# Performance work log

Hardware: AMD Instinct MI355X
Metric: run time of the kernel (lower is better)

The kernel has to match this reference:

```python
import jax, jax.numpy as jnp
import numpy as np

B, S, D, H = 2, 512, 512, 8
HD = D // H  # 64


def setup_inputs() -> dict:
    key = jax.random.key(0)
    ks = jax.random.split(key, 14)
    sd = 1.0 / np.sqrt(D)
    sh = 1.0 / np.sqrt(HD)
    return {
        "query": jax.random.normal(ks[0], (B, S, D), jnp.float32),
        "key_": jax.random.normal(ks[1], (B, S, D), jnp.float32),
        "value": jax.random.normal(ks[2], (B, S, D), jnp.float32),
        "Wq": jax.random.uniform(ks[3], (D, D), jnp.float32, -sd, sd),
        "bq": jax.random.uniform(ks[4], (D,), jnp.float32, -sd, sd),
        "Wk": jax.random.uniform(ks[5], (D, D), jnp.float32, -sd, sd),
        "bk": jax.random.uniform(ks[6], (D,), jnp.float32, -sd, sd),
        "Wv": jax.random.uniform(ks[7], (D, D), jnp.float32, -sd, sd),
        "bv": jax.random.uniform(ks[8], (D,), jnp.float32, -sd, sd),
        "Wo": jax.random.uniform(ks[9], (D, D), jnp.float32, -sd, sd),
        "bo": jax.random.uniform(ks[10], (D,), jnp.float32, -sd, sd),
        "Aq": jax.random.uniform(ks[11], (HD, HD), jnp.float32, -sh, sh),
        "Ak": jax.random.uniform(ks[12], (HD, HD), jnp.float32, -sh, sh),
        "av": jax.random.normal(ks[13], (HD,), jnp.float32) * sh,
    }


def _heads(x):
    b, s, _ = x.shape
    return x.reshape(b, s, H, HD).transpose(0, 2, 1, 3)  # [b,h,s,hd]


def reference(query, key_, value, Wq, bq, Wk, bk, Wv, bv, Wo, bo, Aq, Ak, av):
    q = _heads(query @ Wq + bq)   # [b,h,q,hd]
    k = _heads(key_ @ Wk + bk)    # [b,h,k,hd]
    v = _heads(value @ Wv + bv)   # [b,h,k,hd]
    # additive (Bahdanau-style) scores: tanh(add_q(q)[:,:,:,None]+add_k(k)[:,:,None]) . av
    q_term = (q @ Aq)[:, :, :, None, :]   # [b,h,q,1,hd]
    k_term = (k @ Ak)[:, :, None, :, :]   # [b,h,1,k,hd]
    scores = jnp.einsum('bhqkd,d->bhqk', jnp.tanh(q_term + k_term), av)
    attn_weights = jax.nn.softmax(scores, axis=-1)  # dropout is identity at eval
    ctx = jnp.einsum('bhqk,bhkd->bhqd', attn_weights, v)
    b, _, s, _ = ctx.shape
    ctx = ctx.transpose(0, 2, 1, 3).reshape(b, s, D)
    out = ctx @ Wo + bo
    return out, attn_weights
```

## Files before the change

### kernel.cpp

```cpp
#include <hip/hip_runtime.h>
#include <math.h>

#define Bb 2
#define Ss 512
#define Dd 512
#define Hh 8
#define HDd 64
#define BS (Bb*Ss)

#if __has_builtin(__builtin_amdgcn_exp2f)
#define EXP2F(x) __builtin_amdgcn_exp2f(x)
#else
#define EXP2F(x) exp2f(x)
#endif
#if __has_builtin(__builtin_amdgcn_rcpf)
#define RCPF(x) __builtin_amdgcn_rcpf(x)
#else
#define RCPF(x) (1.0f/(x))
#endif

typedef float v4f __attribute__((ext_vector_type(4)));
typedef short v8s __attribute__((ext_vector_type(8)));

struct HL { short h, l; };

__device__ __forceinline__ HL split1(float x) {
  unsigned u = __builtin_bit_cast(unsigned, x);
  unsigned h = (u + 0x7fffu + ((u >> 16) & 1u)) >> 16;
  float hf = __builtin_bit_cast(float, h << 16);
  float lo = x - hf;
  unsigned ul = __builtin_bit_cast(unsigned, lo);
  unsigned l = (ul + 0x7fffu + ((ul >> 16) & 1u)) >> 16;
  HL r; r.h = (short)h; r.l = (short)l;
  return r;
}

__device__ __forceinline__ void split8p(const float* __restrict__ xp, v8s& ah, v8s& al) {
#pragma unroll
  for (int j = 0; j < 8; j++) {
    const HL r = split1(xp[j]);
    ah[j] = r.h; al[j] = r.l;
  }
}

__device__ __forceinline__ void split8v(float4 x0, float4 x1, v8s& ah, v8s& al) {
  HL r;
  r = split1(x0.x); ah[0] = r.h; al[0] = r.l;
  r = split1(x0.y); ah[1] = r.h; al[1] = r.l;
  r = split1(x0.z); ah[2] = r.h; al[2] = r.l;
  r = split1(x0.w); ah[3] = r.h; al[3] = r.l;
  r = split1(x1.x); ah[4] = r.h; al[4] = r.l;
  r = split1(x1.y); ah[5] = r.h; al[5] = r.l;
  r = split1(x1.z); ah[6] = r.h; al[6] = r.l;
  r = split1(x1.w); ah[7] = r.h; al[7] = r.l;
}

#if __has_builtin(__builtin_amdgcn_global_load_lds)
__device__ __forceinline__ void gl2lds16(const float* g, float* l) {
  __builtin_amdgcn_global_load_lds(
      (const __attribute__((address_space(1))) void*)g,
      (__attribute__((address_space(3))) void*)l, 16, 0, 0);
}
#else
__device__ __forceinline__ void gl2lds16(const float* g, float* l) {
  const int lane = threadIdx.x & 63;
  *(float4*)((char*)l + lane * 16) = *(const float4*)g;
}
#endif

__global__ __launch_bounds__(256) void qkv_all(
    const float* __restrict__ Xq, const float* __restrict__ Xk, const float* __restrict__ Xv,
    const float* __restrict__ Wq, const float* __restrict__ Wk, const float* __restrict__ Wv,
    const float* __restrict__ Wo,
    const float* __restrict__ bq, const float* __restrict__ bk, const float* __restrict__ bv,
    const float* __restrict__ bo,
    const float* __restrict__ Aq, const float* __restrict__ Ak,
    float* __restrict__ EQ, float* __restrict__ EKt, float* __restrict__ Vw,
    short* __restrict__ WoPk, float* __restrict__ outp)
{
  __shared__ __align__(16) short fragH[2][4][64][8];
  __shared__ __align__(16) short fragL[2][4][64][8];
  __shared__ float qs[64][68];
  __shared__ float qs2[16][260];

  const int z = blockIdx.z;
  const float* X    = (z == 0) ? Xq : (z == 1) ? Xk : Xv;
  const float* W    = (z == 0) ? Wq : (z == 1) ? Wk : Wv;
  const float* bias = (z == 0) ? bq : (z == 1) ? bk : bv;
  const int tid = threadIdx.x, l = tid & 63, w = tid >> 6;
  const int lm = l & 15, lq = l >> 4;
  const int h = blockIdx.x;
  const int r0 = blockIdx.y * 64;

  v4f acc[4] = {{0.f,0.f,0.f,0.f},{0.f,0.f,0.f,0.f},{0.f,0.f,0.f,0.f},{0.f,0.f,0.f,0.f}};
  const float* xrow = X + (size_t)(r0 + w * 16 + lm) * Dd + lq * 8;

  for (int kt = 0; kt < 16; ++kt) {
    const int buf = kt & 1;
    const float4 xa0 = *(const float4*)&xrow[kt * 32];
    const float4 xa1 = *(const float4*)&xrow[kt * 32 + 4];
    {
      v8s hh, ll;
#pragma unroll
      for (int j = 0; j < 8; j++) {
        const float x = W[(size_t)(kt * 32 + lq * 8 + j) * Dd + h * 64 + w * 16 + lm];
        const HL r = split1(x);
        hh[j] = r.h; ll[j] = r.l;
      }
      *(v8s*)&fragH[buf][w][l][0] = hh;
      *(v8s*)&fragL[buf][w][l][0] = ll;
    }
    __syncthreads();
    v8s ah, al;
    split8v(xa0, xa1, ah, al);
#pragma unroll
    for (int t = 0; t < 4; t++) {
      const v8s bh = *(const v8s*)&fragH[buf][t][l][0];
      const v8s bl = *(const v8s*)&fragL[buf][t][l][0];
      acc[t] = __builtin_amdgcn_mfma_f32_16x16x32_bf16(ah, bh, acc[t], 0, 0, 0);
      acc[t] = __builtin_amdgcn_mfma_f32_16x16x32_bf16(ah, bl, acc[t], 0, 0, 0);
      acc[t] = __builtin_amdgcn_mfma_f32_16x16x32_bf16(al, bh, acc[t], 0, 0, 0);
    }
  }

  if (z == 2) {
#pragma unroll
    for (int t = 0; t < 4; t++) {
      const int n = h * 64 + t * 16 + lm;
      const float bvv = bias[n];
#pragma unroll
      for (int r = 0; r < 4; r++)
        Vw[(size_t)(r0 + w * 16 + lq * 4 + r) * Dd + n] = acc[t][r] + bvv;
    }
    {
      const int tau = (blockIdx.y * 8 + h) * 4 + w;
      const int nt = tau >> 4, kt = tau & 15;
      v8s hh, ll;
#pragma unroll
      for (int j = 0; j < 8; j++) {
        const float x = Wo[(size_t)(kt * 32 + lq * 8 + j) * Dd + nt * 16 + lm];
        const HL r = split1(x);
        hh[j] = r.h; ll[j] = r.l;
      }
      *(v8s*)&WoPk[((size_t)tau * 64 + l) * 16 + 0] = hh;
      *(v8s*)&WoPk[((size_t)tau * 64 + l) * 16 + 8] = ll;
    }
    for (int i = tid; i < 4096; i += 256) {
      const int rr2 = i >> 6, cc = i & 63;
      outp[(size_t)(r0 + rr2) * Dd + h * 64 + cc] = bo[h * 64 + cc];
    }
    return;
  }

#pragma unroll
  for (int t = 0; t < 4; t++) {
    const int n = h * 64 + t * 16 + lm;
    const float bvv = bias[n];
#pragma unroll
    for (int r = 0; r < 4; r++)
      qs[w * 16 + lq * 4 + r][t * 16 + lm] = acc[t][r] + bvv;
  }
  __syncthreads();

  const float* Am = (z == 0) ? Aq : Ak;
  v4f a2[4] = {{0.f,0.f,0.f,0.f},{0.f,0.f,0.f,0.f},{0.f,0.f,0.f,0.f},{0.f,0.f,0.f,0.f}};
#pragma unroll
  for (int kt2 = 0; kt2 < 2; ++kt2) {
    v8s ah, al;
    split8p(&qs[w * 16 + lm][kt2 * 32 + lq * 8], ah, al);
#pragma unroll
    for (int t2 = 0; t2 < 4; t2++) {
      v8s bh, bl;
#pragma unroll
      for (int j = 0; j < 8; j++) {
        const float x = Am[(kt2 * 32 + lq * 8 + j) * HDd + t2 * 16 + lm]
                        * 2.885390081777927f;
        const HL r = split1(x);
        bh[j] = r.h; bl[j] = r.l;
      }
      a2[t2] = __builtin_amdgcn_mfma_f32_16x16x32_bf16(ah, bh, a2[t2], 0, 0, 0);
      a2[t2] = __builtin_amdgcn_mfma_f32_16x16x32_bf16(ah, bl, a2[t2], 0, 0, 0);
      a2[t2] = __builtin_amdgcn_mfma_f32_16x16x32_bf16(al, bh, a2[t2], 0, 0, 0);
    }
  }

  if (z == 0) {
#pragma unroll
    for (int t2 = 0; t2 < 4; t2++)
#pragma unroll
      for (int rr = 0; rr < 4; rr++)
        EQ[(size_t)(r0 + w * 16 + lq * 4 + rr) * Dd + h * 64 + t2 * 16 + lm] = EXP2F(a2[t2][rr]);
  } else {
#pragma unroll
    for (int t2 = 0; t2 < 4; t2++)
#pragma unroll
      for (int rr = 0; rr < 4; rr++)
        qs2[4 * t2 + (lm >> 2)][(w * 16 + lq * 4 + rr) * 4 + (lm & 3)] = EXP2F(a2[t2][rr]);
    __syncthreads();
    const int b = r0 >> 9;
    const size_t base = (size_t)(b * 8 + h) * 16 * 2048 + (size_t)(r0 & 511) * 4;
#pragma unroll
    for (int i = 0; i < 4; i++) {
      const int f = i * 1024 + tid * 4;
      const int dt = f >> 8, c = f & 255;
      *(float4*)&EKt[base + (size_t)dt * 2048 + c] = *(const float4*)&qs2[dt][c];
    }
  }
}

__device__ __forceinline__ float grp4(v4f e, v4f ek, v4f av4) {
  const v4f one = {1.f, 1.f, 1.f, 1.f};
  const v4f den = e * ek + one;
  const float AB = den.x * den.y;
  const float CD = den.z * den.w;
  const float n1 = __builtin_fmaf(av4.y, den.x, av4.x * den.y);
  const float n2 = __builtin_fmaf(av4.w, den.z, av4.z * den.w);
  const float N = __builtin_fmaf(n2, AB, n1 * CD);
  return N * RCPF(AB * CD);
}

__global__ __launch_bounds__(256) void attn_kernel(
    const float* __restrict__ EQ, const float* __restrict__ EKt,
    const float* __restrict__ V, const float* __restrict__ av,
    const short* __restrict__ WoPk,
    float* __restrict__ attnW, float* __restrict__ outp)
{
  __shared__ __align__(16) float uni[8256];
  __shared__ __align__(16) float eq_s[16][64];
  __shared__ __align__(16) float ctx_s[16][68];
  __shared__ float avn[64];

  const int tid = threadIdx.x, l = tid & 63, w = tid >> 6;
  const int lm = l & 15, lq = l >> 4;
  const int q0 = blockIdx.x * 16;
  const int bh = blockIdx.y;
  const int b = bh >> 3, h = bh & 7;

  {
    const float* eqg = EQ + (size_t)(b * Ss + q0 + w * 4 + lq) * Dd
                       + h * HDd + lm * 4;
    gl2lds16(eqg, &eq_s[w * 4][0]);
  }
  if (tid < 64) avn[tid] = -2.f * av[tid];

  const float* ekbase = EKt + (size_t)bh * 16 * 2048;
  gl2lds16(ekbase + w * 512 + l * 4, &uni[w * 512]);
  gl2lds16(ekbase + w * 512 + 256 + l * 4, &uni[w * 512 + 256]);
  __syncthreads();

  const int qg = w * 4;
  float a[4][8];
#pragma unroll
  for (int j = 0; j < 4; j++)
#pragma unroll
    for (int kg = 0; kg < 8; kg++) a[j][kg] = 0.f;

#pragma unroll 1
  for (int dt = 0; dt < 16; ++dt) {
    const int cb = (dt & 1) * 2048;
    const int nb = 2048 - cb;
    const int dtn = (dt < 15) ? dt + 1 : 15;
    gl2lds16(ekbase + (size_t)dtn * 2048 + w * 512 + l * 4, &uni[nb + w * 512]);
    gl2lds16(ekbase + (size_t)dtn * 2048 + w * 512 + 256 + l * 4, &uni[nb + w * 512 + 256]);

    const v4f av4 = *(const v4f*)&avn[dt * 4];
    const v4f e0 = *(const v4f*)&eq_s[qg + 0][dt * 4];
    const v4f e1 = *(const v4f*)&eq_s[qg + 1][dt * 4];
    const v4f e2 = *(const v4f*)&eq_s[qg + 2][dt * 4];
    const v4f e3 = *(const v4f*)&eq_s[qg + 3][dt * 4];
#pragma unroll
    for (int kg = 0; kg < 8; kg++) {
      const v4f ek = *(const v4f*)&uni[cb + kg * 256 + l * 4];
      a[0][kg] += grp4(e0, ek, av4);
      a[1][kg] += grp4(e1, ek, av4);
      a[2][kg] += grp4(e2, ek, av4);
      a[3][kg] += grp4(e3, ek, av4);
    }
    __syncthreads();
  }

#pragma unroll
  for (int j = 0; j < 4; j++) {
    float m = -1e30f;
#pragma unroll
    for (int kg = 0; kg < 8; kg++) m = fmaxf(m, a[j][kg]);
#pragma unroll
    for (int off = 32; off >= 1; off >>= 1) m = fmaxf(m, __shfl_xor(m, off, 64));
    float s = 0.f;
#pragma unroll
    for (int kg = 0; kg < 8; kg++) {
      a[j][kg] = EXP2F((a[j][kg] - m) * 1.4426950408889634f);
      s += a[j][kg];
    }
#pragma unroll
    for (int off = 32; off >= 1; off >>= 1) s += __shfl_xor(s, off, 64);
    const float inv = RCPF(s);
    float* arow = attnW + ((size_t)bh * Ss + q0 + qg + j) * Ss;
#pragma unroll
    for (int kg = 0; kg < 8; kg++) {
      const float wv = a[j][kg] * inv;
      uni[(qg + j) * 516 + kg * 64 + l] = wv;
      arow[kg * 64 + l] = wv;
    }
  }
  __syncthreads();

  {
    const int rg = (tid >> 4) & 3;
    const int dq = tid & 15;
    const int k0 = w * 128;
    const float* scr0 = &uni[(4 * rg + 0) * 516];
    const float* scr1 = &uni[(4 * rg + 1) * 516];
    const float* scr2 = &uni[(4 * rg + 2) * 516];
    const float* scr3 = &uni[(4 * rg + 3) * 516];
    const float* vb = V + (size_t)b * Ss * Dd + h * HDd + dq * 4;
    v4f o0 = {0.f,0.f,0.f,0.f}, o1 = {0.f,0.f,0.f,0.f};
    v4f o2 = {0.f,0.f,0.f,0.f}, o3 = {0.f,0.f,0.f,0.f};
    for (int kk = k0; kk < k0 + 128; kk += 2) {
      const float2 w0 = *(const float2*)&scr0[kk];
      const float2 w1 = *(const float2*)&scr1[kk];
      const float2 w2 = *(const float2*)&scr2[kk];
      const float2 w3 = *(const float2*)&scr3[kk];
      const v4f va = *(const v4f*)&vb[(size_t)kk * Dd];
      const v4f vz = *(const v4f*)&vb[(size_t)(kk + 1) * Dd];
      o0 += w0.x * va + w0.y * vz;
      o1 += w1.x * va + w1.y * vz;
      o2 += w2.x * va + w2.y * vz;
      o3 += w3.x * va + w3.y * vz;
    }
    __syncthreads();
    *(v4f*)&uni[w * 1024 + (4 * rg + 0) * 64 + dq * 4] = o0;
    *(v4f*)&uni[w * 1024 + (4 * rg + 1) * 64 + dq * 4] = o1;
    *(v4f*)&uni[w * 1024 + (4 * rg + 2) * 64 + dq * 4] = o2;
    *(v4f*)&uni[w * 1024 + (4 * rg + 3) * 64 + dq * 4] = o3;
  }
  __syncthreads();
  {
    const int e = tid * 4;
    const int r = e >> 6, c = e & 63;
    v4f s0 = *(const v4f*)&uni[e];
    s0 += *(const v4f*)&uni[1024 + e];
    s0 += *(const v4f*)&uni[2048 + e];
    s0 += *(const v4f*)&uni[3072 + e];
    *(v4f*)&ctx_s[r][c] = s0;
  }
  __syncthreads();

  {
    v4f oacc[8];
#pragma unroll
    for (int i = 0; i < 8; i++) oacc[i] = (v4f){0.f, 0.f, 0.f, 0.f};
#pragma unroll
    for (int kt2 = 0; kt2 < 2; ++kt2) {
      v8s ah, al;
      split8p(&ctx_s[lm][kt2 * 32 + lq * 8], ah, al);
#pragma unroll
      for (int n8 = 0; n8 < 8; n8++) {
        const int n8i = (n8 + h) & 7;
        const int tau = (w * 8 + n8i) * 16 + 2 * h + kt2;
        const size_t bi = ((size_t)tau * 64 + l) * 16;
        const v8s bh = *(const v8s*)&WoPk[bi + 0];
        const v8s bl = *(const v8s*)&WoPk[bi + 8];
        oacc[n8] = __builtin_amdgcn_mfma_f32_16x16x32_bf16(ah, bh, oacc[n8], 0, 0, 0);
        oacc[n8] = __builtin_amdgcn_mfma_f32_16x16x32_bf16(ah, bl, oacc[n8], 0, 0, 0);
        oacc[n8] = __builtin_amdgcn_mfma_f32_16x16x32_bf16(al, bh, oacc[n8], 0, 0, 0);
      }
    }
#pragma unroll
    for (int n8 = 0; n8 < 8; n8++) {
      const int n8i = (n8 + h) & 7;
      const int n = (w * 8 + n8i) * 16 + lm;
#pragma unroll
      for (int r = 0; r < 4; r++)
        atomicAdd(&outp[(size_t)(b * Ss + q0 + lq * 4 + r) * Dd + n], oacc[n8][r]);
    }
  }
}

extern "C" void kernel_launch(void* const* d_in, const int* in_sizes, int n_in,
                              void* d_out, int out_size, void* d_ws, size_t ws_size,
                              hipStream_t stream) {
  (void)in_sizes; (void)n_in; (void)out_size; (void)ws_size;
  const float* query = (const float*)d_in[0];
  const float* key_  = (const float*)d_in[1];
  const float* value = (const float*)d_in[2];
  const float* Wq    = (const float*)d_in[3];
  const float* bq    = (const float*)d_in[4];
  const float* Wk    = (const float*)d_in[5];
  const float* bk    = (const float*)d_in[6];
  const float* Wv    = (const float*)d_in[7];
  const float* bv    = (const float*)d_in[8];
  const float* Wo    = (const float*)d_in[9];
  const float* bo    = (const float*)d_in[10];
  const float* Aq    = (const float*)d_in[11];
  const float* Ak    = (const float*)d_in[12];
  const float* av    = (const float*)d_in[13];

  float* outp = (float*)d_out;
  float* attn = outp + (size_t)BS * Dd;

  float* ws  = (float*)d_ws;
  float* EQ  = ws;
  float* EKt = ws + (size_t)BS * Dd;
  float* Vw  = ws + 2 * (size_t)BS * Dd;
  short* WoPk = (short*)(ws + 3 * (size_t)BS * Dd);

  qkv_all<<<dim3(8, 16, 3), 256, 0, stream>>>(query, key_, value,
      Wq, Wk, Wv, Wo, bq, bk, bv, bo, Aq, Ak, EQ, EKt, Vw, WoPk, outp);
  attn_kernel<<<dim3(32, 16), 256, 0, stream>>>(EQ, EKt, Vw, av,
      WoPk, attn, outp);
}
```

Measured before the change: 161.9 us.

## Split score work per wave into private EK buffers and drop per-step barriers

Reassigns work in the additive-score loop so each wave handles 8 queries by 256 keys, where before it handled 4 queries by all 512 keys. Each wave now streams its own double-buffered slice of the transposed key term into private LDS regions. The per-iteration __syncthreads is replaced by vmcnt waits, which removes block-wide barriers from the 16-step loop and gives more reuse of each loaded key vector. Softmax now needs a cross-wave combine of partial max and sum through shared memory, and exponentials are recomputed in the write phase. Correctness depends on the raw s_waitcnt encoding and on each lane reading only LDS data it loaded itself.

```diff
diff --git a/kernel.cpp b/kernel.cpp
--- a/kernel.cpp
+++ b/kernel.cpp
@@ -17,6 +17,14 @@
 #define RCPF(x) __builtin_amdgcn_rcpf(x)
 #else
 #define RCPF(x) (1.0f/(x))
+#endif
+
+#if __has_builtin(__builtin_amdgcn_s_waitcnt)
+#define WAIT_VMCNT_4() __builtin_amdgcn_s_waitcnt(0x0F74)
+#define WAIT_VMCNT_0() __builtin_amdgcn_s_waitcnt(0x0F70)
+#else
+#define WAIT_VMCNT_4() __threadfence_block()
+#define WAIT_VMCNT_0() __threadfence_block()
 #endif
 
 typedef float v4f __attribute__((ext_vector_type(4)));
@@ -229,9 +237,11 @@
   __shared__ __align__(16) float eq_s[16][64];
   __shared__ __align__(16) float ctx_s[16][68];
   __shared__ float avn[64];
+  __shared__ float pm[16][2], ps[16][2];
 
   const int tid = threadIdx.x, l = tid & 63, w = tid >> 6;
   const int lm = l & 15, lq = l >> 4;
+  const int wq = w & 1, wk = w >> 1;
   const int q0 = blockIdx.x * 16;
   const int bh = blockIdx.y;
   const int b = bh >> 3, h = bh & 7;
@@ -243,63 +253,74 @@
   }
   if (tid < 64) avn[tid] = -2.f * av[tid];
 
-  const float* ekbase = EKt + (size_t)bh * 16 * 2048;
-  gl2lds16(ekbase + w * 512 + l * 4, &uni[w * 512]);
-  gl2lds16(ekbase + w * 512 + 256 + l * 4, &uni[w * 512 + 256]);
-  __syncthreads();
-
-  const int qg = w * 4;
-  float a[4][8];
+  const float* ekb = EKt + (size_t)bh * 16 * 2048 + wk * 1024;
+  const int dbase = w * 2048;
 #pragma unroll
   for (int j = 0; j < 4; j++)
-#pragma unroll
-    for (int kg = 0; kg < 8; kg++) a[j][kg] = 0.f;
+    gl2lds16(ekb + j * 256 + l * 4, &uni[dbase + j * 256]);
+  __syncthreads();
+
+  float a[8][4];
+#pragma unroll
+  for (int q = 0; q < 8; q++)
+#pragma unroll
+    for (int kg = 0; kg < 4; kg++) a[q][kg] = 0.f;
 
 #pragma unroll 1
   for (int dt = 0; dt < 16; ++dt) {
-    const int cb = (dt & 1) * 2048;
-    const int nb = 2048 - cb;
-    const int dtn = (dt < 15) ? dt + 1 : 15;
-    gl2lds16(ekbase + (size_t)dtn * 2048 + w * 512 + l * 4, &uni[nb + w * 512]);
-    gl2lds16(ekbase + (size_t)dtn * 2048 + w * 512 + 256 + l * 4, &uni[nb + w * 512 + 256]);
+    const int cb = dbase + (dt & 1) * 1024;
+    if (dt < 15) {
+      const int nb = dbase + ((dt + 1) & 1) * 1024;
+      const float* src = ekb + (size_t)(dt + 1) * 2048;
+#pragma unroll
+      for (int j = 0; j < 4; j++)
+        gl2lds16(src + j * 256 + l * 4, &uni[nb + j * 256]);
+      WAIT_VMCNT_4();
+    } else {
+      WAIT_VMCNT_0();
+    }
 
     const v4f av4 = *(const v4f*)&avn[dt * 4];
-    const v4f e0 = *(const v4f*)&eq_s[qg + 0][dt * 4];
-    const v4f e1 = *(const v4f*)&eq_s[qg + 1][dt * 4];
-    const v4f e2 = *(const v4f*)&eq_s[qg + 2][dt * 4];
-    const v4f e3 = *(const v4f*)&eq_s[qg + 3][dt * 4];
-#pragma unroll
-    for (int kg = 0; kg < 8; kg++) {
+    v4f e[8];
+#pragma unroll
+    for (int q = 0; q < 8; q++) e[q] = *(const v4f*)&eq_s[wq * 8 + q][dt * 4];
+#pragma unroll
+    for (int kg = 0; kg < 4; kg++) {
       const v4f ek = *(const v4f*)&uni[cb + kg * 256 + l * 4];
-      a[0][kg] += grp4(e0, ek, av4);
-      a[1][kg] += grp4(e1, ek, av4);
-      a[2][kg] += grp4(e2, ek, av4);
-      a[3][kg] += grp4(e3, ek, av4);
-    }
-    __syncthreads();
-  }
-
-#pragma unroll
-  for (int j = 0; j < 4; j++) {
-    float m = -1e30f;
-#pragma unroll
-    for (int kg = 0; kg < 8; kg++) m = fmaxf(m, a[j][kg]);
+#pragma unroll
+      for (int q = 0; q < 8; q++) a[q][kg] += grp4(e[q], ek, av4);
+    }
+  }
+
+  const float C2 = 1.4426950408889634f;
+#pragma unroll
+  for (int q = 0; q < 8; q++) {
+    const int qq = wq * 8 + q;
+    float m = fmaxf(fmaxf(a[q][0], a[q][1]), fmaxf(a[q][2], a[q][3]));
 #pragma unroll
     for (int off = 32; off >= 1; off >>= 1) m = fmaxf(m, __shfl_xor(m, off, 64));
     float s = 0.f;
 #pragma unroll
-    for (int kg = 0; kg < 8; kg++) {
-      a[j][kg] = EXP2F((a[j][kg] - m) * 1.4426950408889634f);
-      s += a[j][kg];
-    }
+    for (int kg = 0; kg < 4; kg++) s += EXP2F((a[q][kg] - m) * C2);
 #pragma unroll
     for (int off = 32; off >= 1; off >>= 1) s += __shfl_xor(s, off, 64);
+    if (l == 0) { pm[qq][wk] = m; ps[qq][wk] = s; }
+  }
+  __syncthreads();
+
+#pragma unroll
+  for (int q = 0; q < 8; q++) {
+    const int qq = wq * 8 + q;
+    const float m0 = pm[qq][0], m1 = pm[qq][1];
+    const float m = fmaxf(m0, m1);
+    const float s = ps[qq][0] * EXP2F((m0 - m) * C2)
+                  + ps[qq][1] * EXP2F((m1 - m) * C2);
     const float inv = RCPF(s);
-    float* arow = attnW + ((size_t)bh * Ss + q0 + qg + j) * Ss;
-#pragma unroll
-    for (int kg = 0; kg < 8; kg++) {
-      const float wv = a[j][kg] * inv;
-      uni[(qg + j) * 516 + kg * 64 + l] = wv;
+    float* arow = attnW + ((size_t)bh * Ss + q0 + qq) * Ss + wk * 256;
+#pragma unroll
+    for (int kg = 0; kg < 4; kg++) {
+      const float wv = EXP2F((a[q][kg] - m) * C2) * inv;
+      uni[qq * 516 + wk * 256 + kg * 64 + l] = wv;
       arow[kg * 64 + l] = wv;
     }
   }
```

New measurement: 162.1 us. No clear change (+0.1%).

## Fuse projection and attention kernels into one cooperative launch with grid sync

Applied to the files above, without the earlier changes.

Merges the QKV/projection kernel and the attention kernel into a single cooperative kernel of 512 blocks. The first 384 blocks do the projection work, then all blocks wait at a grid-wide barrier and run the attention and output projection. Shared memory is carved from one shared buffer. This removes the second launch and the gap between the two kernels, but adds the cost of a grid barrier and leaves 128 blocks idle during the first phase.

```diff
diff --git a/kernel.cpp b/kernel.cpp
--- a/kernel.cpp
+++ b/kernel.cpp
@@ -1,4 +1,5 @@
 #include <hip/hip_runtime.h>
+#include <hip/hip_cooperative_groups.h>
 #include <math.h>
 
 #define Bb 2
@@ -68,146 +69,6 @@
 }
 #endif
 
-__global__ __launch_bounds__(256) void qkv_all(
-    const float* __restrict__ Xq, const float* __restrict__ Xk, const float* __restrict__ Xv,
-    const float* __restrict__ Wq, const float* __restrict__ Wk, const float* __restrict__ Wv,
-    const float* __restrict__ Wo,
-    const float* __restrict__ bq, const float* __restrict__ bk, const float* __restrict__ bv,
-    const float* __restrict__ bo,
-    const float* __restrict__ Aq, const float* __restrict__ Ak,
-    float* __restrict__ EQ, float* __restrict__ EKt, float* __restrict__ Vw,
-    short* __restrict__ WoPk, float* __restrict__ outp)
-{
-  __shared__ __align__(16) short fragH[2][4][64][8];
-  __shared__ __align__(16) short fragL[2][4][64][8];
-  __shared__ float qs[64][68];
-  __shared__ float qs2[16][260];
-
-  const int z = blockIdx.z;
-  const float* X    = (z == 0) ? Xq : (z == 1) ? Xk : Xv;
-  const float* W    = (z == 0) ? Wq : (z == 1) ? Wk : Wv;
-  const float* bias = (z == 0) ? bq : (z == 1) ? bk : bv;
-  const int tid = threadIdx.x, l = tid & 63, w = tid >> 6;
-  const int lm = l & 15, lq = l >> 4;
-  const int h = blockIdx.x;
-  const int r0 = blockIdx.y * 64;
-
-  v4f acc[4] = {{0.f,0.f,0.f,0.f},{0.f,0.f,0.f,0.f},{0.f,0.f,0.f,0.f},{0.f,0.f,0.f,0.f}};
-  const float* xrow = X + (size_t)(r0 + w * 16 + lm) * Dd + lq * 8;
-
-  for (int kt = 0; kt < 16; ++kt) {
-    const int buf = kt & 1;
-    const float4 xa0 = *(const float4*)&xrow[kt * 32];
-    const float4 xa1 = *(const float4*)&xrow[kt * 32 + 4];
-    {
-      v8s hh, ll;
-#pragma unroll
-      for (int j = 0; j < 8; j++) {
-        const float x = W[(size_t)(kt * 32 + lq * 8 + j) * Dd + h * 64 + w * 16 + lm];
-        const HL r = split1(x);
-        hh[j] = r.h; ll[j] = r.l;
-      }
-      *(v8s*)&fragH[buf][w][l][0] = hh;
-      *(v8s*)&fragL[buf][w][l][0] = ll;
-    }
-    __syncthreads();
-    v8s ah, al;
-    split8v(xa0, xa1, ah, al);
-#pragma unroll
-    for (int t = 0; t < 4; t++) {
-      const v8s bh = *(const v8s*)&fragH[buf][t][l][0];
-      const v8s bl = *(const v8s*)&fragL[buf][t][l][0];
-      acc[t] = __builtin_amdgcn_mfma_f32_16x16x32_bf16(ah, bh, acc[t], 0, 0, 0);
-      acc[t] = __builtin_amdgcn_mfma_f32_16x16x32_bf16(ah, bl, acc[t], 0, 0, 0);
-      acc[t] = __builtin_amdgcn_mfma_f32_16x16x32_bf16(al, bh, acc[t], 0, 0, 0);
-    }
-  }
-
-  if (z == 2) {
-#pragma unroll
-    for (int t = 0; t < 4; t++) {
-      const int n = h * 64 + t * 16 + lm;
-      const float bvv = bias[n];
-#pragma unroll
-      for (int r = 0; r < 4; r++)
-        Vw[(size_t)(r0 + w * 16 + lq * 4 + r) * Dd + n] = acc[t][r] + bvv;
-    }
-    {
-      const int tau = (blockIdx.y * 8 + h) * 4 + w;
-      const int nt = tau >> 4, kt = tau & 15;
-      v8s hh, ll;
-#pragma unroll
-      for (int j = 0; j < 8; j++) {
-        const float x = Wo[(size_t)(kt * 32 + lq * 8 + j) * Dd + nt * 16 + lm];
-        const HL r = split1(x);
-        hh[j] = r.h; ll[j] = r.l;
-      }
-      *(v8s*)&WoPk[((size_t)tau * 64 + l) * 16 + 0] = hh;
-      *(v8s*)&WoPk[((size_t)tau * 64 + l) * 16 + 8] = ll;
-    }
-    for (int i = tid; i < 4096; i += 256) {
-      const int rr2 = i >> 6, cc = i & 63;
-      outp[(size_t)(r0 + rr2) * Dd + h * 64 + cc] = bo[h * 64 + cc];
-    }
-    return;
-  }
-
-#pragma unroll
-  for (int t = 0; t < 4; t++) {
-    const int n = h * 64 + t * 16 + lm;
-    const float bvv = bias[n];
-#pragma unroll
-    for (int r = 0; r < 4; r++)
-      qs[w * 16 + lq * 4 + r][t * 16 + lm] = acc[t][r] + bvv;
-  }
-  __syncthreads();
-
-  const float* Am = (z == 0) ? Aq : Ak;
-  v4f a2[4] = {{0.f,0.f,0.f,0.f},{0.f,0.f,0.f,0.f},{0.f,0.f,0.f,0.f},{0.f,0.f,0.f,0.f}};
-#pragma unroll
-  for (int kt2 = 0; kt2 < 2; ++kt2) {
-    v8s ah, al;
-    split8p(&qs[w * 16 + lm][kt2 * 32 + lq * 8], ah, al);
-#pragma unroll
-    for (int t2 = 0; t2 < 4; t2++) {
-      v8s bh, bl;
-#pragma unroll
-      for (int j = 0; j < 8; j++) {
-        const float x = Am[(kt2 * 32 + lq * 8 + j) * HDd + t2 * 16 + lm]
-                        * 2.885390081777927f;
-        const HL r = split1(x);
-        bh[j] = r.h; bl[j] = r.l;
-      }
-      a2[t2] = __builtin_amdgcn_mfma_f32_16x16x32_bf16(ah, bh, a2[t2], 0, 0, 0);
-      a2[t2] = __builtin_amdgcn_mfma_f32_16x16x32_bf16(ah, bl, a2[t2], 0, 0, 0);
-      a2[t2] = __builtin_amdgcn_mfma_f32_16x16x32_bf16(al, bh, a2[t2], 0, 0, 0);
-    }
-  }
-
-  if (z == 0) {
-#pragma unroll
-    for (int t2 = 0; t2 < 4; t2++)
-#pragma unroll
-      for (int rr = 0; rr < 4; rr++)
-        EQ[(size_t)(r0 + w * 16 + lq * 4 + rr) * Dd + h * 64 + t2 * 16 + lm] = EXP2F(a2[t2][rr]);
-  } else {
-#pragma unroll
-    for (int t2 = 0; t2 < 4; t2++)
-#pragma unroll
-      for (int rr = 0; rr < 4; rr++)
-        qs2[4 * t2 + (lm >> 2)][(w * 16 + lq * 4 + rr) * 4 + (lm & 3)] = EXP2F(a2[t2][rr]);
-    __syncthreads();
-    const int b = r0 >> 9;
-    const size_t base = (size_t)(b * 8 + h) * 16 * 2048 + (size_t)(r0 & 511) * 4;
-#pragma unroll
-    for (int i = 0; i < 4; i++) {
-      const int f = i * 1024 + tid * 4;
-      const int dt = f >> 8, c = f & 255;
-      *(float4*)&EKt[base + (size_t)dt * 2048 + c] = *(const float4*)&qs2[dt][c];
-    }
-  }
-}
-
 __device__ __forceinline__ float grp4(v4f e, v4f ek, v4f av4) {
   const v4f one = {1.f, 1.f, 1.f, 1.f};
   const v4f den = e * ek + one;
@@ -219,160 +80,301 @@
   return N * RCPF(AB * CD);
 }
 
-__global__ __launch_bounds__(256) void attn_kernel(
-    const float* __restrict__ EQ, const float* __restrict__ EKt,
-    const float* __restrict__ V, const float* __restrict__ av,
-    const short* __restrict__ WoPk,
-    float* __restrict__ attnW, float* __restrict__ outp)
+__global__ __launch_bounds__(256) void fused_all(
+    const float* __restrict__ Xq, const float* __restrict__ Xk, const float* __restrict__ Xv,
+    const float* __restrict__ Wq, const float* __restrict__ Wk, const float* __restrict__ Wv,
+    const float* __restrict__ Wo,
+    const float* __restrict__ bq, const float* __restrict__ bk, const float* __restrict__ bv,
+    const float* __restrict__ bo,
+    const float* __restrict__ Aq, const float* __restrict__ Ak, const float* __restrict__ av,
+    float* __restrict__ EQ, float* __restrict__ EKt, float* __restrict__ Vw,
+    short* __restrict__ WoPk, float* __restrict__ attnW, float* __restrict__ outp)
 {
-  __shared__ __align__(16) float uni[8256];
-  __shared__ __align__(16) float eq_s[16][64];
-  __shared__ __align__(16) float ctx_s[16][68];
-  __shared__ float avn[64];
+  __shared__ __align__(16) char smem[50432];
 
   const int tid = threadIdx.x, l = tid & 63, w = tid >> 6;
   const int lm = l & 15, lq = l >> 4;
-  const int q0 = blockIdx.x * 16;
-  const int bh = blockIdx.y;
-  const int b = bh >> 3, h = bh & 7;
+  const int r = blockIdx.x;
+
+  if (r < 384) {
+    short (*fragH)[4][64][8] = (short (*)[4][64][8])(smem);
+    short (*fragL)[4][64][8] = (short (*)[4][64][8])(smem + 8192);
+    float (*qs)[68]   = (float (*)[68])(smem + 16384);
+    float (*qs2)[260] = (float (*)[260])(smem + 33792);
+
+    const int z = r >> 7;
+    const int rem = r & 127;
+    const int h = rem >> 4;
+    const int r0 = (rem & 15) * 64;
+    const float* X    = (z == 0) ? Xq : (z == 1) ? Xk : Xv;
+    const float* W    = (z == 0) ? Wq : (z == 1) ? Wk : Wv;
+    const float* bias = (z == 0) ? bq : (z == 1) ? bk : bv;
+
+    v4f acc[4] = {{0.f,0.f,0.f,0.f},{0.f,0.f,0.f,0.f},{0.f,0.f,0.f,0.f},{0.f,0.f,0.f,0.f}};
+    const float* xrow = X + (size_t)(r0 + w * 16 + lm) * Dd + lq * 8;
+
+    for (int kt = 0; kt < 16; ++kt) {
+      const int buf = kt & 1;
+      const float4 xa0 = *(const float4*)&xrow[kt * 32];
+      const float4 xa1 = *(const float4*)&xrow[kt * 32 + 4];
+      {
+        v8s hh, ll;
+#pragma unroll
+        for (int j = 0; j < 8; j++) {
+          const float x = W[(size_t)(kt * 32 + lq * 8 + j) * Dd + h * 64 + w * 16 + lm];
+          const HL rr = split1(x);
+          hh[j] = rr.h; ll[j] = rr.l;
+        }
+        *(v8s*)&fragH[buf][w][l][0] = hh;
+        *(v8s*)&fragL[buf][w][l][0] = ll;
+      }
+      __syncthreads();
+      v8s ah, al;
+      split8v(xa0, xa1, ah, al);
+#pragma unroll
+      for (int t = 0; t < 4; t++) {
+        const v8s bh = *(const v8s*)&fragH[buf][t][l][0];
+        const v8s bl = *(const v8s*)&fragL[buf][t][l][0];
+        acc[t] = __builtin_amdgcn_mfma_f32_16x16x32_bf16(ah, bh, acc[t], 0, 0, 0);
+        acc[t] = __builtin_amdgcn_mfma_f32_16x16x32_bf16(ah, bl, acc[t], 0, 0, 0);
+        acc[t] = __builtin_amdgcn_mfma_f32_16x16x32_bf16(al, bh, acc[t], 0, 0, 0);
+      }
+    }
+
+    if (z == 2) {
+#pragma unroll
+      for (int t = 0; t < 4; t++) {
+        const int n = h * 64 + t * 16 + lm;
+        const float bvv = bias[n];
+#pragma unroll
+        for (int rr = 0; rr < 4; rr++)
+          Vw[(size_t)(r0 + w * 16 + lq * 4 + rr) * Dd + n] = acc[t][rr] + bvv;
+      }
+      {
+        const int tau = rem * 4 + w;
+        const int nt = tau >> 4, kt = tau & 15;
+        v8s hh, ll;
+#pragma unroll
+        for (int j = 0; j < 8; j++) {
+          const float x = Wo[(size_t)(kt * 32 + lq * 8 + j) * Dd + nt * 16 + lm];
+          const HL rr = split1(x);
+          hh[j] = rr.h; ll[j] = rr.l;
+        }
+        *(v8s*)&WoPk[((size_t)tau * 64 + l) * 16 + 0] = hh;
+        *(v8s*)&WoPk[((size_t)tau * 64 + l) * 16 + 8] = ll;
+      }
+      for (int i = tid; i < 4096; i += 256) {
+        const int rr2 = i >> 6, cc = i & 63;
+        outp[(size_t)(r0 + rr2) * Dd + h * 64 + cc] = bo[h * 64 + cc];
+      }
+    } else {
+#pragma unroll
+      for (int t = 0; t < 4; t++) {
+        const int n = h * 64 + t * 16 + lm;
+        const float bvv = bias[n];
+#pragma unroll
+        for (int rr = 0; rr < 4; rr++)
+          qs[w * 16 + lq * 4 + rr][t * 16 + lm] = acc[t][rr] + bvv;
+      }
+      __syncthreads();
+
+      const float* Am = (z == 0) ? Aq : Ak;
+      v4f a2[4] = {{0.f,0.f,0.f,0.f},{0.f,0.f,0.f,0.f},{0.f,0.f,0.f,0.f},{0.f,0.f,0.f,0.f}};
+#pragma unroll
+      for (int kt2 = 0; kt2 < 2; ++kt2) {
+        v8s ah, al;
+        split8p(&qs[w * 16 + lm][kt2 * 32 + lq * 8], ah, al);
+#pragma unroll
+        for (int t2 = 0; t2 < 4; t2++) {
+          v8s bh, bl;
+#pragma unroll
+          for (int j = 0; j < 8; j++) {
+            const float x = Am[(kt2 * 32 + lq * 8 + j) * HDd + t2 * 16 + lm]
+                            * 2.885390081777927f;
+            const HL rr = split1(x);
+            bh[j] = rr.h; bl[j] = rr.l;
+          }
+          a2[t2] = __builtin_amdgcn_mfma_f32_16x16x32_bf16(ah, bh, a2[t2], 0, 0, 0);
+          a2[t2] = __builtin_amdgcn_mfma_f32_16x16x32_bf16(ah, bl, a2[t2], 0, 0, 0);
+          a2[t2] = __builtin_amdgcn_mfma_f32_16x16x32_bf16(al, bh, a2[t2], 0, 0, 0);
+        }
+      }
+
+      if (z == 0) {
+#pragma unroll
+        for (int t2 = 0; t2 < 4; t2++)
+#pragma unroll
+          for (int rr = 0; rr < 4; rr++)
+            EQ[(size_t)(r0 + w * 16 + lq * 4 + rr) * Dd + h * 64 + t2 * 16 + lm] = EXP2F(a2[t2][rr]);
+      } else {
+#pragma unroll
+        for (int t2 = 0; t2 < 4; t2++)
+#pragma unroll
+          for (int rr = 0; rr < 4; rr++)
+            qs2[4 * t2 + (lm >> 2)][(w * 16 + lq * 4 + rr) * 4 + (lm & 3)] = EXP2F(a2[t2][rr]);
+        __syncthreads();
+        const int b = r0 >> 9;
+        const size_t base = (size_t)(b * 8 + h) * 16 * 2048 + (size_t)(r0 & 511) * 4;
+#pragma unroll
+        for (int i = 0; i < 4; i++) {
+          const int f = i * 1024 + tid * 4;
+          const int dt = f >> 8, c = f & 255;
+          *(float4*)&EKt[base + (size_t)dt * 2048 + c] = *(const float4*)&qs2[dt][c];
+        }
+      }
+    }
+  }
+
+  cooperative_groups::this_grid().sync();
 
   {
-    const float* eqg = EQ + (size_t)(b * Ss + q0 + w * 4 + lq) * Dd
-                       + h * HDd + lm * 4;
-    gl2lds16(eqg, &eq_s[w * 4][0]);
-  }
-  if (tid < 64) avn[tid] = -2.f * av[tid];
-
-  const float* ekbase = EKt + (size_t)bh * 16 * 2048;
-  gl2lds16(ekbase + w * 512 + l * 4, &uni[w * 512]);
-  gl2lds16(ekbase + w * 512 + 256 + l * 4, &uni[w * 512 + 256]);
-  __syncthreads();
-
-  const int qg = w * 4;
-  float a[4][8];
-#pragma unroll
-  for (int j = 0; j < 4; j++)
-#pragma unroll
-    for (int kg = 0; kg < 8; kg++) a[j][kg] = 0.f;
+    float* uni        = (float*)smem;
+    float (*eq_s)[64] = (float (*)[64])(smem + 33024);
+    float (*ctx_s)[68]= (float (*)[68])(smem + 37120);
+    float* avn        = (float*)(smem + 41472);
+
+    const int q0 = (r & 31) * 16;
+    const int bh = r >> 5;
+    const int b = bh >> 3, h = bh & 7;
+
+    {
+      const float* eqg = EQ + (size_t)(b * Ss + q0 + w * 4 + lq) * Dd
+                         + h * HDd + lm * 4;
+      gl2lds16(eqg, &eq_s[w * 4][0]);
+    }
+    if (tid < 64) avn[tid] = -2.f * av[tid];
+
+    const float* ekbase = EKt + (size_t)bh * 16 * 2048;
+    gl2lds16(ekbase + w * 512 + l * 4, &uni[w * 512]);
+    gl2lds16(ekbase + w * 512 + 256 + l * 4, &uni[w * 512 + 256]);
+    __syncthreads();
+
+    const int qg = w * 4;
+    float a[4][8];
+#pragma unroll
+    for (int j = 0; j < 4; j++)
+#pragma unroll
+      for (int kg = 0; kg < 8; kg++) a[j][kg] = 0.f;
 
 #pragma unroll 1
-  for (int dt = 0; dt < 16; ++dt) {
-    const int cb = (dt & 1) * 2048;
-    const int nb = 2048 - cb;
-    const int dtn = (dt < 15) ? dt + 1 : 15;
-    gl2lds16(ekbase + (size_t)dtn * 2048 + w * 512 + l * 4, &uni[nb + w * 512]);
-    gl2lds16(ekbase + (size_t)dtn * 2048 + w * 512 + 256 + l * 4, &uni[nb + w * 512 + 256]);
-
-    const v4f av4 = *(const v4f*)&avn[dt * 4];
-    const v4f e0 = *(const v4f*)&eq_s[qg + 0][dt * 4];
-    const v4f e1 = *(const v4f*)&eq_s[qg + 1][dt * 4];
-    const v4f e2 = *(const v4f*)&eq_s[qg + 2][dt * 4];
-    const v4f e3 = *(const v4f*)&eq_s[qg + 3][dt * 4];
-#pragma unroll
-    for (int kg = 0; kg < 8; kg++) {
-      const v4f ek = *(const v4f*)&uni[cb + kg * 256 + l * 4];
-      a[0][kg] += grp4(e0, ek, av4);
-      a[1][kg] += grp4(e1, ek, av4);
-      a[2][kg] += grp4(e2, ek, av4);
-      a[3][kg] += grp4(e3, ek, av4);
+    for (int dt = 0; dt < 16; ++dt) {
+      const int cb = (dt & 1) * 2048;
+      const int nb = 2048 - cb;
+      const int dtn = (dt < 15) ? dt + 1 : 15;
+      gl2lds16(ekbase + (size_t)dtn * 2048 + w * 512 + l * 4, &uni[nb + w * 512]);
+      gl2lds16(ekbase + (size_t)dtn * 2048 + w * 512 + 256 + l * 4, &uni[nb + w * 512 + 256]);
+
+      const v4f av4 = *(const v4f*)&avn[dt * 4];
+      const v4f e0 = *(const v4f*)&eq_s[qg + 0][dt * 4];
+      const v4f e1 = *(const v4f*)&eq_s[qg + 1][dt * 4];
+      const v4f e2 = *(const v4f*)&eq_s[qg + 2][dt * 4];
+      const v4f e3 = *(const v4f*)&eq_s[qg + 3][dt * 4];
+#pragma unroll
+      for (int kg = 0; kg < 8; kg++) {
+        const v4f ek = *(const v4f*)&uni[cb + kg * 256 + l * 4];
+        a[0][kg] += grp4(e0, ek, av4);
+        a[1][kg] += grp4(e1, ek, av4);
+        a[2][kg] += grp4(e2, ek, av4);
+        a[3][kg] += grp4(e3, ek, av4);
+      }
+      __syncthreads();
+    }
+
+#pragma unroll
+    for (int j = 0; j < 4; j++) {
+      float m = -1e30f;
+#pragma unroll
+      for (int kg = 0; kg < 8; kg++) m = fmaxf(m, a[j][kg]);
+#pragma unroll
+      for (int off = 32; off >= 1; off >>= 1) m = fmaxf(m, __shfl_xor(m, off, 64));
+      float s = 0.f;
+#pragma unroll
+      for (int kg = 0; kg < 8; kg++) {
+        a[j][kg] = EXP2F((a[j][kg] - m) * 1.4426950408889634f);
+        s += a[j][kg];
+      }
+#pragma unroll
+      for (int off = 32; off >= 1; off >>= 1) s += __shfl_xor(s, off, 64);
+      const float inv = RCPF(s);
+      float* arow = attnW + ((size_t)bh * Ss + q0 + qg + j) * Ss;
+#pragma unroll
+      for (int kg = 0; kg < 8; kg++) {
+        const float wv = a[j][kg] * inv;
+        uni[(qg + j) * 516 + kg * 64 + l] = wv;
+        arow[kg * 64 + l] = wv;
+      }
     }
     __syncthreads();
-  }
-
-#pragma unroll
-  for (int j = 0; j < 4; j++) {
-    float m = -1e30f;
-#pragma unroll
-    for (int kg = 0; kg < 8; kg++) m = fmaxf(m, a[j][kg]);
-#pragma unroll
-    for (int off = 32; off >= 1; off >>= 1) m = fmaxf(m, __shfl_xor(m, off, 64));
-    float s = 0.f;
-#pragma unroll
-    for (int kg = 0; kg < 8; kg++) {
-      a[j][kg] = EXP2F((a[j][kg] - m) * 1.4426950408889634f);
-      s += a[j][kg];
-    }
-#pragma unroll
-    for (int off = 32; off >= 1; off >>= 1) s += __shfl_xor(s, off, 64);
-    const float inv = RCPF(s);
-    float* arow = attnW + ((size_t)bh * Ss + q0 + qg + j) * Ss;
-#pragma unroll
-    for (int kg = 0; kg < 8; kg++) {
-      const float wv = a[j][kg] * inv;
-      uni[(qg + j) * 516 + kg * 64 + l] = wv;
-      arow[kg * 64 + l] = wv;
-    }
-  }
-  __syncthreads();
-
-  {
-    const int rg = (tid >> 4) & 3;
-    const int dq = tid & 15;
-    const int k0 = w * 128;
-    const float* scr0 = &uni[(4 * rg + 0) * 516];
-    const float* scr1 = &uni[(4 * rg + 1) * 516];
-    const float* scr2 = &uni[(4 * rg + 2) * 516];
-    const float* scr3 = &uni[(4 * rg + 3) * 516];
-    const float* vb = V + (size_t)b * Ss * Dd + h * HDd + dq * 4;
-    v4f o0 = {0.f,0.f,0.f,0.f}, o1 = {0.f,0.f,0.f,0.f};
-    v4f o2 = {0.f,0.f,0.f,0.f}, o3 = {0.f,0.f,0.f,0.f};
-    for (int kk = k0; kk < k0 + 128; kk += 2) {
-      const float2 w0 = *(const float2*)&scr0[kk];
-      const float2 w1 = *(const float2*)&scr1[kk];
-      const float2 w2 = *(const float2*)&scr2[kk];
-      const float2 w3 = *(const float2*)&scr3[kk];
-      const v4f va = *(const v4f*)&vb[(size_t)kk * Dd];
-      const v4f vz = *(const v4f*)&vb[(size_t)(kk + 1) * Dd];
-      o0 += w0.x * va + w0.y * vz;
-      o1 += w1.x * va + w1.y * vz;
-      o2 += w2.x * va + w2.y * vz;
-      o3 += w3.x * va + w3.y * vz;
+
+    {
+      const int rg = (tid >> 4) & 3;
+      const int dq = tid & 15;
+      const int k0 = w * 128;
+      const float* scr0 = &uni[(4 * rg + 0) * 516];
+      const float* scr1 = &uni[(4 * rg + 1) * 516];
+      const float* scr2 = &uni[(4 * rg + 2) * 516];
+      const float* scr3 = &uni[(4 * rg + 3) * 516];
+      const float* vb = Vw + (size_t)b * Ss * Dd + h * HDd + dq * 4;
+      v4f o0 = {0.f,0.f,0.f,0.f}, o1 = {0.f,0.f,0.f,0.f};
+      v4f o2 = {0.f,0.f,0.f,0.f}, o3 = {0.f,0.f,0.f,0.f};
+      for (int kk = k0; kk < k0 + 128; kk += 2) {
+        const float2 w0 = *(const float2*)&scr0[kk];
+        const float2 w1 = *(const float2*)&scr1[kk];
+        const float2 w2 = *(const float2*)&scr2[kk];
+        const float2 w3 = *(const float2*)&scr3[kk];
+        const v4f va = *(const v4f*)&vb[(size_t)kk * Dd];
+        const v4f vz = *(const v4f*)&vb[(size_t)(kk + 1) * Dd];
+        o0 += w0.x * va + w0.y * vz;
+        o1 += w1.x * va + w1.y * vz;
+        o2 += w2.x * va + w2.y * vz;
+        o3 += w3.x * va + w3.y * vz;
+      }
+      __syncthreads();
+      *(v4f*)&uni[w * 1024 + (4 * rg + 0) * 64 + dq * 4] = o0;
+      *(v4f*)&uni[w * 1024 + (4 * rg + 1) * 64 + dq * 4] = o1;
+      *(v4f*)&uni[w * 1024 + (4 * rg + 2) * 64 + dq * 4] = o2;
+      *(v4f*)&uni[w * 1024 + (4 * rg + 3) * 64 + dq * 4] = o3;
     }
     __syncthreads();
-    *(v4f*)&uni[w * 1024 + (4 * rg + 0) * 64 + dq * 4] = o0;
-    *(v4f*)&uni[w * 1024 + (4 * rg + 1) * 64 + dq * 4] = o1;
-    *(v4f*)&uni[w * 1024 + (4 * rg + 2) * 64 + dq * 4] = o2;
-    *(v4f*)&uni[w * 1024 + (4 * rg + 3) * 64 + dq * 4] = o3;
-  }
-  __syncthreads();
-  {
-    const int e = tid * 4;
-    const int r = e >> 6, c = e & 63;
-    v4f s0 = *(const v4f*)&uni[e];
-    s0 += *(const v4f*)&uni[1024 + e];
-    s0 += *(const v4f*)&uni[2048 + e];
-    s0 += *(const v4f*)&uni[3072 + e];
-    *(v4f*)&ctx_s[r][c] = s0;
-  }
-  __syncthreads();
-
-  {
-    v4f oacc[8];
-#pragma unroll
-    for (int i = 0; i < 8; i++) oacc[i] = (v4f){0.f, 0.f, 0.f, 0.f};
-#pragma unroll
-    for (int kt2 = 0; kt2 < 2; ++kt2) {
-      v8s ah, al;
-      split8p(&ctx_s[lm][kt2 * 32 + lq * 8], ah, al);
+    {
+      const int e = tid * 4;
+      const int rr = e >> 6, c = e & 63;
+      v4f s0 = *(const v4f*)&uni[e];
+      s0 += *(const v4f*)&uni[1024 + e];
+      s0 += *(const v4f*)&uni[2048 + e];
+      s0 += *(const v4f*)&uni[3072 + e];
+      *(v4f*)&ctx_s[rr][c] = s0;
+    }
+    __syncthreads();
+
+    {
+      v4f oacc[8];
+#pragma unroll
+      for (int i = 0; i < 8; i++) oacc[i] = (v4f){0.f, 0.f, 0.f, 0.f};
+#pragma unroll
+      for (int kt2 = 0; kt2 < 2; ++kt2) {
+        v8s ah, al;
+        split8p(&ctx_s[lm][kt2 * 32 + lq * 8], ah, al);
+#pragma unroll
+        for (int n8 = 0; n8 < 8; n8++) {
+          const int n8i = (n8 + h) & 7;
+          const int tau = (w * 8 + n8i) * 16 + 2 * h + kt2;
+          const size_t bi = ((size_t)tau * 64 + l) * 16;
+          const v8s bh = *(const v8s*)&WoPk[bi + 0];
+          const v8s bl = *(const v8s*)&WoPk[bi + 8];
+          oacc[n8] = __builtin_amdgcn_mfma_f32_16x16x32_bf16(ah, bh, oacc[n8], 0, 0, 0);
+          oacc[n8] = __builtin_amdgcn_mfma_f32_16x16x32_bf16(ah, bl, oacc[n8], 0, 0, 0);
+          oacc[n8] = __builtin_amdgcn_mfma_f32_16x16x32_bf16(al, bh, oacc[n8], 0, 0, 0);
+        }
+      }
 #pragma unroll
       for (int n8 = 0; n8 < 8; n8++) {
         const int n8i = (n8 + h) & 7;
-        const int tau = (w * 8 + n8i) * 16 + 2 * h + kt2;
-        const size_t bi = ((size_t)tau * 64 + l) * 16;
-        const v8s bh = *(const v8s*)&WoPk[bi + 0];
-        const v8s bl = *(const v8s*)&WoPk[bi + 8];
-        oacc[n8] = __builtin_amdgcn_mfma_f32_16x16x32_bf16(ah, bh, oacc[n8], 0, 0, 0);
-        oacc[n8] = __builtin_amdgcn_mfma_f32_16x16x32_bf16(ah, bl, oacc[n8], 0, 0, 0);
-        oacc[n8] = __builtin_amdgcn_mfma_f32_16x16x32_bf16(al, bh, oacc[n8], 0, 0, 0);
-      }
-    }
-#pragma unroll
-    for (int n8 = 0; n8 < 8; n8++) {
-      const int n8i = (n8 + h) & 7;
-      const int n = (w * 8 + n8i) * 16 + lm;
-#pragma unroll
-      for (int r = 0; r < 4; r++)
-        atomicAdd(&outp[(size_t)(b * Ss + q0 + lq * 4 + r) * Dd + n], oacc[n8][r]);
+        const int n = (w * 8 + n8i) * 16 + lm;
+#pragma unroll
+        for (int rr = 0; rr < 4; rr++)
+          atomicAdd(&outp[(size_t)(b * Ss + q0 + lq * 4 + rr) * Dd + n], oacc[n8][rr]);
+      }
     }
   }
 }
@@ -405,8 +407,14 @@
   float* Vw  = ws + 2 * (size_t)BS * Dd;
   short* WoPk = (short*)(ws + 3 * (size_t)BS * Dd);
 
-  qkv_all<<<dim3(8, 16, 3), 256, 0, stream>>>(query, key_, value,
-      Wq, Wk, Wv, Wo, bq, bk, bv, bo, Aq, Ak, EQ, EKt, Vw, WoPk, outp);
-  attn_kernel<<<dim3(32, 16), 256, 0, stream>>>(EQ, EKt, Vw, av,
-      WoPk, attn, outp);
-}
+  void* args[] = {
+    (void*)&query, (void*)&key_, (void*)&value,
+    (void*)&Wq, (void*)&Wk, (void*)&Wv, (void*)&Wo,
+    (void*)&bq, (void*)&bk, (void*)&bv, (void*)&bo,
+    (void*)&Aq, (void*)&Ak, (void*)&av,
+    (void*)&EQ, (void*)&EKt, (void*)&Vw,
+    (void*)&WoPk, (void*)&attn, (void*)&outp
+  };
+  hipLaunchCooperativeKernel((void*)fused_all, dim3(512), dim3(256),
+                             args, 0, stream);
+}
```

After: 243.9 us. 50.7% more time.
